# Performance work log

Measured on AMD Instinct MI355X. Metric: run time of the kernel, lower is better.

## Reference

```python
import jax, jax.numpy as jnp
import numpy as np

B, L_TXT, L_IMG = 1, 256, 2048
D_MODEL, HEADS, DIM_HEAD = 2048, 16, 128
S = L_TXT + L_IMG
QMAX = 127.0  # int8 symmetric
SM_SCALE = 1.0 / float(np.sqrt(DIM_HEAD))


def quant_act(x):
    # dynamic per-tensor symmetric int8 fake-quant with straight-through estimator
    scale = jnp.maximum(jnp.max(jnp.abs(x)) / QMAX, 1e-8)
    q = jnp.clip(jnp.round(x / scale), -QMAX, QMAX) * scale
    return x + jax.lax.stop_gradient(q - x)


def quant_weight(w):
    # per-output-channel symmetric int8 fake-quant (STE)
    scale = jnp.maximum(jnp.max(jnp.abs(w), axis=1, keepdims=True) / QMAX, 1e-8)
    q = jnp.clip(jnp.round(w / scale), -QMAX, QMAX) * scale
    return w + jax.lax.stop_gradient(q - w)


def qlinear(x, w, b):
    return x @ quant_weight(w).T + b


def rmsnorm(x, w, eps=1e-6):
    var = jnp.mean(jnp.square(x), axis=-1, keepdims=True)
    return x * jax.lax.rsqrt(var + eps) * w


def apply_rope(x, cos, sin):
    # diffusers apply_rotary_emb, use_real with interleaved (real, imag) pairs
    xr = x.reshape(*x.shape[:-1], -1, 2)
    rot = jnp.stack([-xr[..., 1], xr[..., 0]], axis=-1).reshape(x.shape)
    return x * cos + rot * sin


def heads_split(x):
    # [B, L, H*D] -> [B, H, L, D]
    return x.reshape(B, -1, HEADS, DIM_HEAD).transpose(0, 2, 1, 3)


def setup_inputs() -> dict:
    key = jax.random.key(0)
    ks = jax.random.split(key, 12)
    inp = {
        'hidden_states': jax.random.normal(ks[0], (B, L_IMG, D_MODEL), jnp.float32),
        'encoder_hidden_states': jax.random.normal(ks[1], (B, L_TXT, D_MODEL), jnp.float32),
    }
    freqs = 1.0 / (10000.0 ** (jnp.arange(0, DIM_HEAD, 2, dtype=jnp.float32) / DIM_HEAD))
    ang = jnp.arange(S, dtype=jnp.float32)[:, None] * freqs[None, :]  # [S, D/2]
    inp['rope_cos'] = jnp.repeat(jnp.cos(ang), 2, axis=-1)  # [S, D]
    inp['rope_sin'] = jnp.repeat(jnp.sin(ang), 2, axis=-1)
    wn = ['wq', 'wk', 'wv', 'w_add_q', 'w_add_k', 'w_add_v', 'w_out', 'w_add_out']
    bn = ['bq', 'bk', 'bv', 'b_add_q', 'b_add_k', 'b_add_v', 'b_out', 'b_add_out']
    for i, (w, b) in enumerate(zip(wn, bn)):
        inp[w] = jax.random.normal(ks[2 + i], (D_MODEL, D_MODEL), jnp.float32) * 0.02
        inp[b] = jnp.zeros((D_MODEL,), jnp.float32)
    for n in ['norm_q_w', 'norm_k_w', 'norm_added_q_w', 'norm_added_k_w']:
        inp[n] = jnp.ones((DIM_HEAD,), jnp.float32)
    return inp


def reference(hidden_states, encoder_hidden_states, rope_cos, rope_sin,
              wq, bq, wk, bk, wv, bv,
              w_add_q, b_add_q, w_add_k, b_add_k, w_add_v, b_add_v,
              w_out, b_out, w_add_out, b_add_out,
              norm_q_w, norm_k_w, norm_added_q_w, norm_added_k_w):
    # image-token branch
    h = quant_act(hidden_states)
    q = heads_split(qlinear(h, wq, bq))
    k = heads_split(qlinear(h, wk, bk))
    v = heads_split(qlinear(h, wv, bv))
    q = quant_act(rmsnorm(q, norm_q_w))
    k = quant_act(rmsnorm(k, norm_k_w))
    v = quant_act(v)
    # text-token (encoder) branch
    e = quant_act(encoder_hidden_states)
    eq = heads_split(qlinear(e, w_add_q, b_add_q))
    ek = heads_split(qlinear(e, w_add_k, b_add_k))
    ev = heads_split(qlinear(e, w_add_v, b_add_v))
    eq = quant_act(rmsnorm(eq, norm_added_q_w))
    ek = quant_act(rmsnorm(ek, norm_added_k_w))
    ev = quant_act(ev)
    # joint sequence: [text; image]
    q = jnp.concatenate([eq, q], axis=2)
    k = jnp.concatenate([ek, k], axis=2)
    v = jnp.concatenate([ev, v], axis=2)
    cos = rope_cos[None, None]
    sin = rope_sin[None, None]
    q = apply_rope(q, cos, sin)
    k = apply_rope(k, cos, sin)
    scores = jnp.einsum('bhqd,bhkd->bhqk', q, k) * SM_SCALE
    probs = jax.nn.softmax(scores, axis=-1)
    out = jnp.einsum('bhqk,bhkd->bhqd', probs, v)
    out = out.transpose(0, 2, 1, 3).reshape(B, S, HEADS * DIM_HEAD)
    out = quant_act(out)
    enc, img = out[:, :L_TXT], out[:, L_TXT:]
    img = qlinear(img, w_out, b_out)
    enc = qlinear(enc, w_add_out, b_add_out)
    return (img, enc)
```

## Files before the change

kernel.cpp:

```cpp
#include <hip/hip_runtime.h>

constexpr int L_TXT = 256, L_IMG = 2048, SEQ = 2304;
constexpr int DM = 2048, NH = 16, DH = 128;
constexpr int NSPLIT = 4;
constexpr int SSTR = 32;

typedef __attribute__((ext_vector_type(8))) __bf16 bf16x8;
typedef __attribute__((ext_vector_type(4))) float f32x4;

__device__ __forceinline__ float ldin(const void* p, size_t i, int bf) {
  return bf ? (float)((const __bf16*)p)[i] : ((const float*)p)[i];
}
__device__ __forceinline__ float slot_scale(const unsigned* s) {
  return fmaxf(__uint_as_float(*s) / 127.0f, 1e-8f);
}
__device__ __forceinline__ float qclamp(float x, float sc) {
  float q = rintf(x / sc);
  return fminf(fmaxf(q, -127.0f), 127.0f);
}
__device__ __forceinline__ float block_allmax_n(float v) {
  #pragma unroll
  for (int off = 32; off; off >>= 1) v = fmaxf(v, __shfl_xor(v, off));
  __shared__ float sm[16];
  int nw = blockDim.x >> 6;
  __syncthreads();
  if ((threadIdx.x & 63) == 0) sm[threadIdx.x >> 6] = v;
  __syncthreads();
  float m = sm[0];
  for (int i = 1; i < nw; i++) m = fmaxf(m, sm[i]);
  return m;
}

__global__ void detect_k(const void* cosp, int* flag) {
  if (threadIdx.x == 0) *flag = (((const unsigned short*)cosp)[0] != 0) ? 1 : 0;
}

struct Ptrs8 { const void* p[8]; };

__global__ void quant_weights_k(Ptrs8 win, __bf16* __restrict__ wq, float* __restrict__ scales,
                                const int* __restrict__ flagp) {
  const int bf = *flagp;
  int row = blockIdx.x, mat = blockIdx.y, t = threadIdx.x;
  float v[8];
  if (bf) {
    union { int4 q; __bf16 h[8]; } u;
    u.q = ((const int4*)((const __bf16*)win.p[mat] + (size_t)row * DM))[t];
    #pragma unroll
    for (int j = 0; j < 8; j++) v[j] = (float)u.h[j];
  } else {
    const float4* p = (const float4*)((const float*)win.p[mat] + (size_t)row * DM);
    float4 a = p[t * 2], b = p[t * 2 + 1];
    v[0]=a.x; v[1]=a.y; v[2]=a.z; v[3]=a.w; v[4]=b.x; v[5]=b.y; v[6]=b.z; v[7]=b.w;
  }
  float m = 0.f;
  #pragma unroll
  for (int j = 0; j < 8; j++) m = fmaxf(m, fabsf(v[j]));
  m = block_allmax_n(m);
  float sc = fmaxf(m / 127.0f, 1e-8f);
  if (t == 0) scales[mat * DM + row] = sc;
  union { int4 q; __bf16 h[8]; } o;
  #pragma unroll
  for (int j = 0; j < 8; j++) o.h[j] = (__bf16)qclamp(v[j], sc);
  ((int4*)(wq + (size_t)mat * DM * DM + (size_t)row * DM))[t] = o.q;
}
__global__ void weight_scales_k(Ptrs8 win, float* __restrict__ scales, const int* __restrict__ flagp) {
  const int bf = *flagp;
  int row = blockIdx.x, mat = blockIdx.y, t = threadIdx.x;
  float m = 0.f;
  for (int c = t; c < DM; c += 256) m = fmaxf(m, fabsf(ldin(win.p[mat], (size_t)row * DM + c, bf)));
  m = block_allmax_n(m);
  if (t == 0) scales[mat * DM + row] = fmaxf(m / 127.0f, 1e-8f);
}

__global__ void absmax_he_k(const void* __restrict__ hs, const void* __restrict__ es,
                            unsigned* s0, unsigned* s1, const int* __restrict__ flagp) {
  const int bf = *flagp;
  const int n18 = L_IMG * DM / 8, n28 = L_TXT * DM / 8;
  float m1 = 0.f, m2 = 0.f;
  for (int i = blockIdx.x * 256 + threadIdx.x; i < n18 + n28; i += gridDim.x * 256) {
    bool h = i < n18;
    const void* src = h ? hs : es;
    int j = h ? i : i - n18;
    float lm = 0.f;
    if (bf) {
      union { int4 q; __bf16 x[8]; } u; u.q = ((const int4*)src)[j];
      #pragma unroll
      for (int k = 0; k < 8; k++) lm = fmaxf(lm, fabsf((float)u.x[k]));
    } else {
      const float4* p = (const float4*)src;
      float4 a = p[j * 2], b = p[j * 2 + 1];
      lm = fmaxf(fmaxf(fmaxf(fabsf(a.x), fabsf(a.y)), fmaxf(fabsf(a.z), fabsf(a.w))),
                 fmaxf(fmaxf(fabsf(b.x), fabsf(b.y)), fmaxf(fabsf(b.z), fabsf(b.w))));
    }
    if (h) m1 = fmaxf(m1, lm); else m2 = fmaxf(m2, lm);
  }
  m1 = block_allmax_n(m1);
  __syncthreads();
  m2 = block_allmax_n(m2);
  if (threadIdx.x == 0) { atomicMax(s0, __float_as_uint(m1)); atomicMax(s1, __float_as_uint(m2)); }
}

__global__ void quant_he_k(const void* __restrict__ hs, const void* __restrict__ es,
                           const unsigned* __restrict__ slots, __bf16* __restrict__ hqo,
                           __bf16* __restrict__ eqo, const int* __restrict__ flagp) {
  const int bf = *flagp;
  const int n18 = L_IMG * DM / 8, n28 = L_TXT * DM / 8;
  float sc0 = slot_scale(slots), sc1 = slot_scale(slots + SSTR);
  for (int i = blockIdx.x * 256 + threadIdx.x; i < n18 + n28; i += gridDim.x * 256) {
    bool h = i < n18;
    const void* src = h ? hs : es;
    int j = h ? i : i - n18;
    float sc = h ? sc0 : sc1;
    float v[8];
    if (bf) {
      union { int4 q; __bf16 x[8]; } u; u.q = ((const int4*)src)[j];
      #pragma unroll
      for (int k = 0; k < 8; k++) v[k] = (float)u.x[k];
    } else {
      const float4* p = (const float4*)src;
      float4 a = p[j * 2], b = p[j * 2 + 1];
      v[0]=a.x; v[1]=a.y; v[2]=a.z; v[3]=a.w; v[4]=b.x; v[5]=b.y; v[6]=b.z; v[7]=b.w;
    }
    union { int4 q; __bf16 x[8]; } o;
    #pragma unroll
    for (int k = 0; k < 8; k++) o.x[k] = (__bf16)qclamp(v[k], sc);
    ((int4*)(h ? hqo : eqo))[j] = o.q;
  }
}

__global__ void quant_f32x8_k(const float* __restrict__ x, int n8,
                              const unsigned* __restrict__ slot, __bf16* __restrict__ out) {
  float sc = slot_scale(slot);
  for (int i = blockIdx.x * 256 + threadIdx.x; i < n8; i += gridDim.x * 256) {
    float4 a = ((const float4*)x)[i * 2], b = ((const float4*)x)[i * 2 + 1];
    union { int4 q; __bf16 h[8]; } o;
    o.h[0]=(__bf16)qclamp(a.x,sc); o.h[1]=(__bf16)qclamp(a.y,sc);
    o.h[2]=(__bf16)qclamp(a.z,sc); o.h[3]=(__bf16)qclamp(a.w,sc);
    o.h[4]=(__bf16)qclamp(b.x,sc); o.h[5]=(__bf16)qclamp(b.y,sc);
    o.h[6]=(__bf16)qclamp(b.z,sc); o.h[7]=(__bf16)qclamp(b.w,sc);
    ((int4*)out)[i] = o.q;
  }
}
__global__ void absmax_f32_k(const float* __restrict__ x, int n, unsigned* slot) {
  float m = 0.f;
  for (int i = blockIdx.x * 256 + threadIdx.x; i < n; i += gridDim.x * 256)
    m = fmaxf(m, fabsf(x[i]));
  m = block_allmax_n(m);
  if (threadIdx.x == 0) atomicMax(slot, __float_as_uint(m));
}

__global__ void rms_absmax_v_k(float* __restrict__ qf, float* __restrict__ kf, float* __restrict__ vf,
                               const void* nq, const void* naq, const void* nk, const void* nak,
                               unsigned* __restrict__ slots, const int* __restrict__ flagp) {
  const int bf = *flagp;
  const int t = threadIdx.x, lane = t & 63, wave = t >> 6;
  float wqt0 = ldin(naq, lane, bf), wqt1 = ldin(naq, lane + 64, bf);
  float wqi0 = ldin(nq,  lane, bf), wqi1 = ldin(nq,  lane + 64, bf);
  float wkt0 = ldin(nak, lane, bf), wkt1 = ldin(nak, lane + 64, bf);
  float wki0 = ldin(nk,  lane, bf), wki1 = ldin(nk,  lane + 64, bf);
  const int NR = NH * SEQ;
  float mx[6] = {0.f, 0.f, 0.f, 0.f, 0.f, 0.f};
  for (int row = blockIdx.x * 16 + wave; row < 3 * NR; row += gridDim.x * 16) {
    int tns = row / NR, r2 = row - tns * NR;
    int s = r2 % SEQ; bool txt = s < L_TXT;
    float* p = (tns == 0 ? qf : tns == 1 ? kf : vf) + (size_t)r2 * DH;
    float v0 = p[lane], v1 = p[lane + 64];
    if (tns < 2) {
      float ss = v0 * v0 + v1 * v1;
      #pragma unroll
      for (int off = 32; off; off >>= 1) ss += __shfl_xor(ss, off);
      float r = rsqrtf(ss * (1.0f / 128.0f) + 1e-6f);
      float w0, w1;
      if (tns == 0) { w0 = txt ? wqt0 : wqi0; w1 = txt ? wqt1 : wqi1; }
      else          { w0 = txt ? wkt0 : wki0; w1 = txt ? wkt1 : wki1; }
      v0 *= r * w0; v1 *= r * w1;
      p[lane] = v0; p[lane + 64] = v1;
    }
    int idx = tns * 2 + (txt ? 0 : 1);
    mx[idx] = fmaxf(mx[idx], fmaxf(fabsf(v0), fabsf(v1)));
  }
  #pragma unroll
  for (int off = 32; off; off >>= 1)
    #pragma unroll
    for (int j = 0; j < 6; j++) mx[j] = fmaxf(mx[j], __shfl_xor(mx[j], off));
  __shared__ float smx[16][6];
  if (lane == 0)
    #pragma unroll
    for (int j = 0; j < 6; j++) smx[wave][j] = mx[j];
  __syncthreads();
  if (t == 0) {
    #pragma unroll
    for (int j = 0; j < 6; j++) {
      float m = smx[0][j];
      for (int i = 1; i < 16; i++) m = fmaxf(m, smx[i][j]);
      atomicMax(slots + (2 + j) * SSTR, __float_as_uint(m));
    }
  }
}

__global__ void rope2_k(const float* __restrict__ qf, const float* __restrict__ kf,
                        const void* cosb, const void* sinb, const unsigned* __restrict__ slots,
                        __bf16* __restrict__ qb, __bf16* __restrict__ kb, const int* __restrict__ flagp) {
  const int bf = *flagp;
  const int NP = NH * SEQ * 64;
  for (int i = blockIdx.x * 256 + threadIdx.x; i < 2 * NP; i += gridDim.x * 256) {
    int tns = i >= NP;
    int j = i - tns * NP;
    int pr = j & 63, rowg = j >> 6;
    int s = rowg % SEQ;
    const float* src = tns ? kf : qf;
    __bf16* dst = tns ? kb : qb;
    float sc = slot_scale(slots + (tns ? 4 : 2) * SSTR + (s < L_TXT ? 0 : SSTR));
    size_t base = (size_t)rowg * DH + pr * 2;
    float2 x2 = *(const float2*)(src + base);
    float q0 = qclamp(x2.x, sc) * sc, q1 = qclamp(x2.y, sc) * sc;
    float c0 = ldin(cosb, s * DH + 2 * pr, bf), c1 = ldin(cosb, s * DH + 2 * pr + 1, bf);
    float s0 = ldin(sinb, s * DH + 2 * pr, bf), s1 = ldin(sinb, s * DH + 2 * pr + 1, bf);
    dst[base]     = (__bf16)(q0 * c0 - q1 * s0);
    dst[base + 1] = (__bf16)(q1 * c1 + q0 * s1);
  }
}

__global__ void quant_transpose_v_k(const float* __restrict__ v, const unsigned* __restrict__ slots,
                                    __bf16* __restrict__ vt) {
  __shared__ float tile[64][65];
  int t = threadIdx.x;
  int s0 = blockIdx.x * 64, d0 = blockIdx.y * 64, h = blockIdx.z;
  #pragma unroll
  for (int i = 0; i < 16; i++) {
    int r = i * 4 + (t >> 6), c = t & 63;
    tile[r][c] = v[((size_t)(h * SEQ) + s0 + r) * DH + d0 + c];
  }
  __syncthreads();
  float sc = slot_scale(slots + (s0 < L_TXT ? 6 : 7) * SSTR);
  #pragma unroll
  for (int i = 0; i < 16; i++) {
    int d = i * 4 + (t >> 6), s = t & 63;
    float q = qclamp(tile[s][d], sc) * sc;
    vt[((size_t)(h * DH) + d0 + d) * SEQ + s0 + s] = (__bf16)q;
  }
}

struct GemmArgs {
  const __bf16 *hq, *eq, *attnq;
  const __bf16* wqp;
  const void* Wraw[8];
  const float* wsc;
  const void* bias[8];
  float* outs[3];
  void* dout;
  const unsigned* slots;
  const int* flagp;
};
template<int MODE, int QW>
__global__ __launch_bounds__(256, 2)
void gemm_f(GemmArgs a) {
  const int bf = *a.flagp;
  constexpr int K = DM;
  __shared__ __bf16 As[128][72];
  __shared__ __bf16 Ws[128][72];
  const int t = threadIdx.x, lane = t & 63, wave = t >> 6;
  const int l15 = lane & 15, quad = lane >> 4;
  const int n0 = blockIdx.x * 128, y = blockIdx.y;
  int mat, outrow; const __bf16* A; const unsigned* aslot;
  if (MODE == 0) {
    bool txt = y < 2;
    mat = blockIdx.z + (txt ? 3 : 0);
    A = (txt ? a.eq : a.hq) + (size_t)(txt ? y * 128 : (y - 2) * 128) * K;
    outrow = y * 128;
    aslot = a.slots + (txt ? SSTR : 0);
  } else {
    bool img = y < 16;
    mat = img ? 6 : 7;
    A = a.attnq + (size_t)(img ? L_TXT + y * 128 : (y - 16) * 128) * K;
    outrow = img ? y * 128 : L_IMG + (y - 16) * 128;
    aslot = a.slots + 8 * SSTR;
  }
  const __bf16* Wq = QW ? a.wqp + (size_t)mat * DM * DM : nullptr;
  const void* Wr = a.Wraw[mat];
  const float* wrow = a.wsc + mat * DM;
  int wm = (wave & 1) * 64, wn = (wave >> 1) * 64;
  f32x4 acc[4][4] = {};
  int sr = t >> 3, sc = (t & 7) * 8;
  float wsc4[4];
  if (!QW) {
    #pragma unroll
    for (int p = 0; p < 4; p++) wsc4[p] = wrow[n0 + p * 32 + sr];
  }
  for (int k0 = 0; k0 < K; k0 += 64) {
    __syncthreads();
    #pragma unroll
    for (int p = 0; p < 4; p++) {
      int r = p * 32 + sr;
      *(int4*)&As[r][sc] = *(const int4*)&A[(size_t)r * K + k0 + sc];
      if (QW) {
        *(int4*)&Ws[r][sc] = *(const int4*)&Wq[(size_t)(n0 + r) * K + k0 + sc];
      } else {
        union { bf16x8 v; __bf16 h[8]; } q;
        if (bf) {
          union { int4 v; __bf16 h[8]; } u;
          u.v = *(const int4*)((const __bf16*)Wr + (size_t)(n0 + r) * K + k0 + sc);
          #pragma unroll
          for (int j = 0; j < 8; j++) q.h[j] = (__bf16)qclamp((float)u.h[j], wsc4[p]);
        } else {
          const float* wp = (const float*)Wr + (size_t)(n0 + r) * K + k0 + sc;
          float4 x = *(const float4*)wp, z = *(const float4*)(wp + 4);
          q.h[0]=(__bf16)qclamp(x.x,wsc4[p]); q.h[1]=(__bf16)qclamp(x.y,wsc4[p]);
          q.h[2]=(__bf16)qclamp(x.z,wsc4[p]); q.h[3]=(__bf16)qclamp(x.w,wsc4[p]);
          q.h[4]=(__bf16)qclamp(z.x,wsc4[p]); q.h[5]=(__bf16)qclamp(z.y,wsc4[p]);
          q.h[6]=(__bf16)qclamp(z.z,wsc4[p]); q.h[7]=(__bf16)qclamp(z.w,wsc4[p]);
        }
        *(bf16x8*)&Ws[r][sc] = q.v;
      }
    }
    __syncthreads();
    #pragma unroll
    for (int kk = 0; kk < 64; kk += 32) {
      bf16x8 af[4], bfr[4];
      #pragma unroll
      for (int i = 0; i < 4; i++) {
        af[i]  = *(const bf16x8*)&As[wm + i * 16 + l15][kk + quad * 8];
        bfr[i] = *(const bf16x8*)&Ws[wn + i * 16 + l15][kk + quad * 8];
      }
      #pragma unroll
      for (int i = 0; i < 4; i++)
        #pragma unroll
        for (int j = 0; j < 4; j++)
          acc[i][j] = __builtin_amdgcn_mfma_f32_16x16x32_bf16(af[i], bfr[j], acc[i][j], 0, 0, 0);
    }
  }
  float asc = slot_scale(aslot);
  #pragma unroll
  for (int j = 0; j < 4; j++) {
    int gn = n0 + wn + j * 16 + l15;
    float wsb = wrow[gn] * asc;
    float bv = ldin(a.bias[mat], gn, bf);
    #pragma unroll
    for (int i = 0; i < 4; i++)
      #pragma unroll
      for (int r = 0; r < 4; r++) {
        int gm = wm + i * 16 + quad * 4 + r;
        float val = acc[i][j][r] * wsb + bv;
        if (MODE == 0) {
          a.outs[blockIdx.z][(size_t)(gn >> 7) * (SEQ * DH) + (size_t)(outrow + gm) * DH + (gn & 127)] = val;
        } else {
          size_t idx = (size_t)(outrow + gm) * DM + gn;
          if (bf) ((__bf16*)a.dout)[idx] = (__bf16)val; else ((float*)a.dout)[idx] = val;
        }
      }
  }
}

template<int SPLIT>
__global__ __launch_bounds__(256, 3)
void flash_attn_k(const __bf16* __restrict__ Qb, const __bf16* __restrict__ Kb,
                  const __bf16* __restrict__ Vt, float* __restrict__ O,
                  float* __restrict__ Op, float* __restrict__ Mp, float* __restrict__ Lp) {
  __shared__ __align__(16) char smem[19456 + 18432];
  auto Ks = (__bf16(*)[152])smem;
  auto Ps = (__bf16(*)[72])smem;
  auto Vs = (__bf16(*)[72])(smem + 19456);
  const int t = threadIdx.x, lane = t & 63, wave = t >> 6;
  const int l15 = lane & 15, quad = lane >> 4;
  const int h = blockIdx.y, s0 = blockIdx.x * 128, qr = wave * 32;
  const float fscale = 0.08838834764831845f * 1.4426950408889634f;

  bf16x8 qf[2][4];
  #pragma unroll
  for (int mi = 0; mi < 2; mi++)
    #pragma unroll
    for (int kk = 0; kk < 4; kk++)
      qf[mi][kk] = *(const bf16x8*)&Qb[(size_t)(h * SEQ + s0 + qr + mi * 16 + l15) * DH + kk * 32 + quad * 8];

  f32x4 accO[2][8] = {};
  float m_st[2][4], l_st[2][4];
  #pragma unroll
  for (int mi = 0; mi < 2; mi++)
    #pragma unroll
    for (int r = 0; r < 4; r++) { m_st[mi][r] = -1e30f; l_st[mi][r] = 0.f; }

  const int ktb = SPLIT ? blockIdx.z * (SEQ / 64 / NSPLIT) : 0;
  const int kte = SPLIT ? ktb + (SEQ / 64 / NSPLIT) : SEQ / 64;
  for (int kt = ktb; kt < kte; kt++) {
    __syncthreads();
    #pragma unroll
    for (int p = 0; p < 4; p++) {
      int r = p * 16 + (t >> 4), c = (t & 15) * 8;
      *(int4*)&Ks[r][c] = *(const int4*)&Kb[(size_t)(h * SEQ + kt * 64 + r) * DH + c];
    }
    #pragma unroll
    for (int p = 0; p < 4; p++) {
      int r = p * 32 + (t >> 3), c = (t & 7) * 8;
      *(int4*)&Vs[r][c] = *(const int4*)&Vt[(size_t)(h * DH + r) * SEQ + kt * 64 + c];
    }
    __syncthreads();

    f32x4 accS[2][4] = {};
    #pragma unroll
    for (int kk = 0; kk < 4; kk++) {
      bf16x8 bk[4];
      #pragma unroll
      for (int ni = 0; ni < 4; ni++)
        bk[ni] = *(const bf16x8*)&Ks[ni * 16 + l15][kk * 32 + quad * 8];
      #pragma unroll
      for (int mi = 0; mi < 2; mi++)
        #pragma unroll
        for (int ni = 0; ni < 4; ni++)
          accS[mi][ni] = __builtin_amdgcn_mfma_f32_16x16x32_bf16(qf[mi][kk], bk[ni], accS[mi][ni], 0, 0, 0);
    }

    float al[2][4];
    #pragma unroll
    for (int mi = 0; mi < 2; mi++)
      #pragma unroll
      for (int r = 0; r < 4; r++) {
        float rm = fmaxf(fmaxf(accS[mi][0][r], accS[mi][1][r]), fmaxf(accS[mi][2][r], accS[mi][3][r]));
        #pragma unroll
        for (int off = 8; off > 0; off >>= 1) rm = fmaxf(rm, __shfl_xor(rm, off));
        float mn = fmaxf(m_st[mi][r], rm);
        al[mi][r] = exp2f((m_st[mi][r] - mn) * fscale);
        m_st[mi][r] = mn;
      }
    #pragma unroll
    for (int mi = 0; mi < 2; mi++)
      #pragma unroll
      for (int r = 0; r < 4; r++) {
        float rs = 0.f;
        #pragma unroll
        for (int ni = 0; ni < 4; ni++) {
          float pv = exp2f((accS[mi][ni][r] - m_st[mi][r]) * fscale);
          accS[mi][ni][r] = pv;
          rs += pv;
        }
        #pragma unroll
        for (int off = 8; off > 0; off >>= 1) rs += __shfl_xor(rs, off);
        l_st[mi][r] = l_st[mi][r] * al[mi][r] + rs;
      }
    #pragma unroll
    for (int mi = 0; mi < 2; mi++)
      #pragma unroll
      for (int di = 0; di < 8; di++)
        #pragma unroll
        for (int r = 0; r < 4; r++)
          accO[mi][di][r] *= al[mi][r];
    __syncthreads();
    #pragma unroll
    for (int mi = 0; mi < 2; mi++)
      #pragma unroll
      for (int ni = 0; ni < 4; ni++)
        #pragma unroll
        for (int r = 0; r < 4; r++)
          Ps[qr + mi * 16 + quad * 4 + r][ni * 16 + l15] = (__bf16)accS[mi][ni][r];
    #pragma unroll
    for (int kk2 = 0; kk2 < 2; kk2++) {
      bf16x8 pa[2], vb[8];
      #pragma unroll
      for (int mi = 0; mi < 2; mi++)
        pa[mi] = *(const bf16x8*)&Ps[qr + mi * 16 + l15][kk2 * 32 + quad * 8];
      #pragma unroll
      for (int di = 0; di < 8; di++)
        vb[di] = *(const bf16x8*)&Vs[di * 16 + l15][kk2 * 32 + quad * 8];
      #pragma unroll
      for (int mi = 0; mi < 2; mi++)
        #pragma unroll
        for (int di = 0; di < 8; di++)
          accO[mi][di] = __builtin_amdgcn_mfma_f32_16x16x32_bf16(pa[mi], vb[di], accO[mi][di], 0, 0, 0);
    }
  }
  if (SPLIT) {
    const size_t SP = (size_t)NH * SEQ * DH;
    const int sp = blockIdx.z;
    #pragma unroll
    for (int mi = 0; mi < 2; mi++)
      #pragma unroll
      for (int r = 0; r < 4; r++) {
        int gs = s0 + qr + mi * 16 + quad * 4 + r;
        size_t ib = sp * SP + ((size_t)h * SEQ + gs) * DH;
        if (l15 == 0) {
          Mp[(size_t)sp * NH * SEQ + h * SEQ + gs] = m_st[mi][r];
          Lp[(size_t)sp * NH * SEQ + h * SEQ + gs] = l_st[mi][r];
        }
        #pragma unroll
        for (int di = 0; di < 8; di++)
          Op[ib + di * 16 + l15] = accO[mi][di][r];
      }
  } else {
    #pragma unroll
    for (int mi = 0; mi < 2; mi++)
      #pragma unroll
      for (int r = 0; r < 4; r++) {
        float inv = 1.0f / l_st[mi][r];
        int gs = s0 + qr + mi * 16 + quad * 4 + r;
        #pragma unroll
        for (int di = 0; di < 8; di++)
          O[(size_t)gs * DM + h * DH + di * 16 + l15] = accO[mi][di][r] * inv;
      }
  }
}

__global__ void flash_combine_k(const float* __restrict__ Op, const float* __restrict__ Mp,
                                const float* __restrict__ Lp, float* __restrict__ O,
                                unsigned* __restrict__ slot8) {
  const float fscale = 0.08838834764831845f * 1.4426950408889634f;
  const int t = threadIdx.x, lane = t & 63, w = t >> 6;
  const size_t SP = (size_t)NH * SEQ * DH, MR = (size_t)NH * SEQ;
  float lm = 0.f;
  for (int row = blockIdx.x * 16 + w; row < NH * SEQ; row += gridDim.x * 16) {
    float m0 = Mp[row], m1 = Mp[MR + row], m2 = Mp[2 * MR + row], m3 = Mp[3 * MR + row];
    float M = fmaxf(fmaxf(m0, m1), fmaxf(m2, m3));
    float w0 = exp2f((m0 - M) * fscale), w1 = exp2f((m1 - M) * fscale);
    float w2 = exp2f((m2 - M) * fscale), w3 = exp2f((m3 - M) * fscale);
    float inv = 1.0f / (Lp[row] * w0 + Lp[MR + row] * w1 + Lp[2 * MR + row] * w2 + Lp[3 * MR + row] * w3);
    int h = row / SEQ, s = row % SEQ;
    size_t ob = (size_t)s * DM + h * DH, ib = (size_t)row * DH;
    #pragma unroll
    for (int j = 0; j < 2; j++) {
      int d = lane + j * 64;
      float v = (Op[ib + d] * w0 + Op[SP + ib + d] * w1 +
                 Op[2 * SP + ib + d] * w2 + Op[3 * SP + ib + d] * w3) * inv;
      O[ob + d] = v;
      lm = fmaxf(lm, fabsf(v));
    }
  }
  lm = block_allmax_n(lm);
  if (t == 0) atomicMax(slot8, __float_as_uint(lm));
}

extern "C" void kernel_launch(void* const* d_in, const int* in_sizes, int n_in,
                              void* d_out, int out_size, void* d_ws, size_t ws_size,
                              hipStream_t stream) {
  (void)in_sizes; (void)n_in; (void)out_size;
  const void* hs   = d_in[0];
  const void* es   = d_in[1];
  const void* cosb = d_in[2];
  const void* sinb = d_in[3];
  const void* W[8]; const void* Bv[8];
  for (int i = 0; i < 8; i++) { W[i] = d_in[4 + 2 * i]; Bv[i] = d_in[5 + 2 * i]; }
  const void* nq  = d_in[20];
  const void* nk  = d_in[21];
  const void* naq = d_in[22];
  const void* nak = d_in[23];

  char* ws = (char*)d_ws;
  size_t off = 0;
  auto take = [&](size_t b) { char* p = ws + off; off += (b + 255) & ~(size_t)255; return p; };
  const size_t T = (size_t)NH * SEQ * DH * 4;

  unsigned* slots = (unsigned*)take(16 * SSTR * 4);
  int* flagp = (int*)(slots + 15 * SSTR);
  float* wsc = (float*)take(8ull * DM * 4);

  size_t here = off;
  size_t need_base  = 4 * T + T + 3 * (T / 2) + 2 * ((size_t)NSPLIT * NH * SEQ * 4 + 256) + 1024;
  bool do_split = here + need_base <= ws_size;
  size_t region_sz = do_split ? 4 * T : 3 * T;

  char* region = take(region_sz);
  float* qf = (float*)region;
  float* kf = (float*)(region + T);
  float* vf = (float*)(region + 2 * T);
  float* Opart = (float*)region;
  __bf16* attnq = (__bf16*)region;
  char* attnfR = take(T);
  __bf16* hq = (__bf16*)attnfR;
  __bf16* eq = (__bf16*)(attnfR + (size_t)L_IMG * DM * 2);
  float* attnf = (float*)attnfR;
  __bf16* qb  = (__bf16*)take(T / 2);
  __bf16* kb  = (__bf16*)take(T / 2);
  __bf16* vtb = (__bf16*)take(T / 2);
  float* Mpart = (float*)take((size_t)NSPLIT * NH * SEQ * 4);
  float* Lpart = (float*)take((size_t)NSPLIT * NH * SEQ * 4);
  bool do_prequant = (off + 8ull * DM * DM * 2 + 256 <= ws_size);
  __bf16* wq = do_prequant ? (__bf16*)take(8ull * DM * DM * 2) : nullptr;

  hipMemsetAsync(slots, 0, 16 * SSTR * 4, stream);
  detect_k<<<1, 64, 0, stream>>>(cosb, flagp);

  Ptrs8 win;
  for (int i = 0; i < 8; i++) win.p[i] = W[i];
  if (do_prequant)
    quant_weights_k<<<dim3(DM, 8), 256, 0, stream>>>(win, wq, wsc, flagp);
  else
    weight_scales_k<<<dim3(DM, 8), 256, 0, stream>>>(win, wsc, flagp);

  absmax_he_k<<<512, 256, 0, stream>>>(hs, es, slots, slots + SSTR, flagp);
  quant_he_k<<<1024, 256, 0, stream>>>(hs, es, slots, hq, eq, flagp);

  GemmArgs ga;
  ga.hq = hq; ga.eq = eq; ga.attnq = attnq; ga.wqp = wq;
  for (int i = 0; i < 8; i++) { ga.Wraw[i] = W[i]; ga.bias[i] = Bv[i]; }
  ga.wsc = wsc; ga.outs[0] = qf; ga.outs[1] = kf; ga.outs[2] = vf;
  ga.dout = d_out; ga.slots = slots; ga.flagp = flagp;

  if (do_prequant)
    gemm_f<0, 1><<<dim3(16, 18, 3), 256, 0, stream>>>(ga);
  else
    gemm_f<0, 0><<<dim3(16, 18, 3), 256, 0, stream>>>(ga);

  rms_absmax_v_k<<<256, 1024, 0, stream>>>(qf, kf, vf, nq, naq, nk, nak, slots, flagp);
  rope2_k<<<1024, 256, 0, stream>>>(qf, kf, cosb, sinb, slots, qb, kb, flagp);
  quant_transpose_v_k<<<dim3(SEQ / 64, DH / 64, NH), 256, 0, stream>>>(vf, slots, vtb);

  if (do_split) {
    flash_attn_k<1><<<dim3(SEQ / 128, NH, NSPLIT), 256, 0, stream>>>(qb, kb, vtb, nullptr,
                                                                     Opart, Mpart, Lpart);
    flash_combine_k<<<288, 1024, 0, stream>>>(Opart, Mpart, Lpart, attnf, slots + 8 * SSTR);
  } else {
    flash_attn_k<0><<<dim3(SEQ / 128, NH), 256, 0, stream>>>(qb, kb, vtb, attnf,
                                                             nullptr, nullptr, nullptr);
    absmax_f32_k<<<256, 256, 0, stream>>>(attnf, SEQ * DM, slots + 8 * SSTR);
  }
  quant_f32x8_k<<<1024, 256, 0, stream>>>(attnf, SEQ * DM / 8, slots + 8 * SSTR, attnq);

  if (do_prequant)
    gemm_f<1, 1><<<dim3(16, 18), 256, 0, stream>>>(ga);
  else
    gemm_f<1, 0><<<dim3(16, 18), 256, 0, stream>>>(ga);
}
```

Before: 696.6 us.

## Prefetch next K/V tile into registers and give P its own LDS buffer

The flash attention loop now loads the next K/V tile from global memory into registers while the current tile is being computed, then stores it to LDS at the top of the next iteration. The P (probabilities) buffer moves to its own LDS region so it no longer aliases K, which removes one block barrier per iteration. s_setprio is raised around the MFMA sections to favour matrix issue. In exchange, LDS use grows, extra registers hold the prefetched tile, and launch bounds drop from 3 to 2 blocks per CU, so occupancy falls.

```diff
diff --git a/kernel.cpp b/kernel.cpp
--- a/kernel.cpp
+++ b/kernel.cpp
@@ -352,14 +352,14 @@
 }
 
 template<int SPLIT>
-__global__ __launch_bounds__(256, 3)
+__global__ __launch_bounds__(256, 2)
 void flash_attn_k(const __bf16* __restrict__ Qb, const __bf16* __restrict__ Kb,
                   const __bf16* __restrict__ Vt, float* __restrict__ O,
                   float* __restrict__ Op, float* __restrict__ Mp, float* __restrict__ Lp) {
-  __shared__ __align__(16) char smem[19456 + 18432];
+  __shared__ __align__(16) char smem[19456 + 18432 + 18432];
   auto Ks = (__bf16(*)[152])smem;
-  auto Ps = (__bf16(*)[72])smem;
   auto Vs = (__bf16(*)[72])(smem + 19456);
+  auto Ps = (__bf16(*)[72])(smem + 19456 + 18432);
   const int t = threadIdx.x, lane = t & 63, wave = t >> 6;
   const int l15 = lane & 15, quad = lane >> 4;
   const int h = blockIdx.y, s0 = blockIdx.x * 128, qr = wave * 32;
@@ -381,21 +381,37 @@
 
   const int ktb = SPLIT ? blockIdx.z * (SEQ / 64 / NSPLIT) : 0;
   const int kte = SPLIT ? ktb + (SEQ / 64 / NSPLIT) : SEQ / 64;
+
+  const int krr = t >> 4, krc = (t & 15) * 8;
+  const int vrr = t >> 3, vrc = (t & 7) * 8;
+  int4 kreg[4], vreg[4];
+  #pragma unroll
+  for (int p = 0; p < 4; p++)
+    kreg[p] = *(const int4*)&Kb[(size_t)(h * SEQ + ktb * 64 + p * 16 + krr) * DH + krc];
+  #pragma unroll
+  for (int p = 0; p < 4; p++)
+    vreg[p] = *(const int4*)&Vt[(size_t)(h * DH + p * 32 + vrr) * SEQ + ktb * 64 + vrc];
+
   for (int kt = ktb; kt < kte; kt++) {
-    __syncthreads();
-    #pragma unroll
-    for (int p = 0; p < 4; p++) {
-      int r = p * 16 + (t >> 4), c = (t & 15) * 8;
-      *(int4*)&Ks[r][c] = *(const int4*)&Kb[(size_t)(h * SEQ + kt * 64 + r) * DH + c];
-    }
-    #pragma unroll
-    for (int p = 0; p < 4; p++) {
-      int r = p * 32 + (t >> 3), c = (t & 7) * 8;
-      *(int4*)&Vs[r][c] = *(const int4*)&Vt[(size_t)(h * DH + r) * SEQ + kt * 64 + c];
-    }
-    __syncthreads();
+    asm volatile("s_waitcnt lgkmcnt(0)" ::: "memory");
+    __builtin_amdgcn_s_barrier();
+    #pragma unroll
+    for (int p = 0; p < 4; p++) *(int4*)&Ks[p * 16 + krr][krc] = kreg[p];
+    #pragma unroll
+    for (int p = 0; p < 4; p++) *(int4*)&Vs[p * 32 + vrr][vrc] = vreg[p];
+    if (kt + 1 < kte) {
+      #pragma unroll
+      for (int p = 0; p < 4; p++)
+        kreg[p] = *(const int4*)&Kb[(size_t)(h * SEQ + (kt + 1) * 64 + p * 16 + krr) * DH + krc];
+      #pragma unroll
+      for (int p = 0; p < 4; p++)
+        vreg[p] = *(const int4*)&Vt[(size_t)(h * DH + p * 32 + vrr) * SEQ + (kt + 1) * 64 + vrc];
+    }
+    asm volatile("s_waitcnt lgkmcnt(0)" ::: "memory");
+    __builtin_amdgcn_s_barrier();
 
     f32x4 accS[2][4] = {};
+    __builtin_amdgcn_s_setprio(1);
     #pragma unroll
     for (int kk = 0; kk < 4; kk++) {
       bf16x8 bk[4];
@@ -408,6 +424,7 @@
         for (int ni = 0; ni < 4; ni++)
           accS[mi][ni] = __builtin_amdgcn_mfma_f32_16x16x32_bf16(qf[mi][kk], bk[ni], accS[mi][ni], 0, 0, 0);
     }
+    __builtin_amdgcn_s_setprio(0);
 
     float al[2][4];
     #pragma unroll
@@ -443,7 +460,6 @@
         #pragma unroll
         for (int r = 0; r < 4; r++)
           accO[mi][di][r] *= al[mi][r];
-    __syncthreads();
     #pragma unroll
     for (int mi = 0; mi < 2; mi++)
       #pragma unroll
@@ -451,6 +467,7 @@
         #pragma unroll
         for (int r = 0; r < 4; r++)
           Ps[qr + mi * 16 + quad * 4 + r][ni * 16 + l15] = (__bf16)accS[mi][ni][r];
+    __builtin_amdgcn_s_setprio(1);
     #pragma unroll
     for (int kk2 = 0; kk2 < 2; kk2++) {
       bf16x8 pa[2], vb[8];
@@ -466,6 +483,7 @@
         for (int di = 0; di < 8; di++)
           accO[mi][di] = __builtin_amdgcn_mfma_f32_16x16x32_bf16(pa[mi], vb[di], accO[mi][di], 0, 0, 0);
     }
+    __builtin_amdgcn_s_setprio(0);
   }
   if (SPLIT) {
     const size_t SP = (size_t)NH * SEQ * DH;
```

Result: faster. 677.9 us (-2.7%).
